# Kernel tuning notes

Hardware: AMD Instinct MI355X
Metric: run time of the kernel (lower is better)

The kernel has to match this reference:

```python
import jax, jax.numpy as jnp
import numpy as np

N_NODES = 8192
N_EDGES = 65536
MUL = 16          # multiplicity of 0e and 1o irreps
NB = 16           # num_radial_basis
HID = 16          # num_radial_dimension
MAX_RADIUS = 5.0
SQRT3 = float(np.sqrt(3.0))


def soft_unit_step(x):
    # e3nn.math.soft_unit_step: exp(-1/x) for x>0 else 0 (grad-safe where)
    safe = jnp.where(x > 0, x, 1.0)
    return jnp.where(x > 0, jnp.exp(-1.0 / safe), 0.0)


def setup_inputs() -> dict:
    key = jax.random.key(0)
    ks = jax.random.split(key, 12)
    f_in = jax.random.normal(ks[0], (N_NODES, 4 * MUL), jnp.float32)
    edge_vec = jax.random.normal(ks[1], (N_EDGES, 3), jnp.float32) * 1.5
    edge_src = jax.random.randint(ks[2], (N_EDGES,), 0, N_NODES)
    edge_dst = jax.random.randint(ks[3], (N_EDGES,), 0, N_NODES)
    Wq0 = jax.random.normal(ks[4], (MUL, MUL), jnp.float32)
    Wq1 = jax.random.normal(ks[5], (MUL, MUL), jnp.float32)
    Wk1 = jax.random.normal(ks[6], (NB, HID), jnp.float32)
    Wk2 = jax.random.normal(ks[7], (HID, 4 * MUL * MUL), jnp.float32)
    Wv1 = jax.random.normal(ks[8], (NB, HID), jnp.float32)
    Wv2 = jax.random.normal(ks[9], (HID, 4 * MUL * MUL), jnp.float32)
    Wd0 = jax.random.normal(ks[10], (MUL, MUL), jnp.float32)
    Wd1 = jax.random.normal(ks[11], (MUL, MUL), jnp.float32)
    return dict(f_in=f_in, edge_vec=edge_vec, edge_src=edge_src, edge_dst=edge_dst,
                Wq0=Wq0, Wq1=Wq1, Wk1=Wk1, Wk2=Wk2, Wv1=Wv1, Wv2=Wv2, Wd0=Wd0, Wd1=Wd1)


def _forward(f_in, edge_vec, edge_src, edge_dst,
             Wq0, Wq1, Wk1, Wk2, Wv1, Wv2, Wd0, Wd1):
    f0 = f_in[:, :MUL]                         # [N, MUL]    0e scalars
    f1 = f_in[:, MUL:].reshape(-1, MUL, 3)     # [N, MUL, 3] 1o vectors

    r = jnp.linalg.norm(edge_vec, axis=1)      # [E]
    u = edge_vec / r[:, None]
    sh1 = SQRT3 * u                            # Y_1, component norm (|Y1|^2 = 3); Y_0 = 1

    # soft_one_hot_linspace, basis='smooth_finite', cutoff=True, * sqrt(NB)
    values = jnp.linspace(0.0, MAX_RADIUS, NB + 2)
    step = values[1] - values[0]
    diff = (r[:, None] - values[1:-1]) / step
    C = 1.14136 * float(np.exp(2.0))
    rb = (C * soft_unit_step(diff + 1.0) * soft_unit_step(1.0 - diff)) * np.sqrt(NB)

    edge_cut = soft_unit_step(10.0 * (1.0 - r / MAX_RADIUS))  # [E]

    def mlp(x, W1, W2):  # e3nn FullyConnectedNet with fan-in normalization
        h = jax.nn.silu(x @ (W1 / np.sqrt(NB)))
        return h @ (W2 / np.sqrt(HID))

    wk = mlp(rb, Wk1, Wk2).reshape(-1, 4, MUL, MUL)  # per-edge TP weights
    wv = mlp(rb, Wv1, Wv2).reshape(-1, 4, MUL, MUL)

    # h_q: per-irrep linear
    q0 = f0 @ Wq0 / np.sqrt(MUL)
    q1 = jnp.einsum('nic,io->noc', f1, Wq1) / np.sqrt(MUL)

    x0 = f0[edge_src]   # [E, MUL]
    x1 = f1[edge_src]   # [E, MUL, 3]

    def fctp(w):
        # FullyConnectedTensorProduct (16x0e+16x1o) x (0e+1o) -> (16x0e+16x1o)
        # 4 paths: 0x0->0, 1x1->0 (dot/sqrt3), 0x1->1, 1x0->1
        a = 1.0 / np.sqrt(2 * MUL)
        o0 = jnp.einsum('eij,ei->ej', w[:, 0], x0) \
           + jnp.einsum('eij,eic,ec->ej', w[:, 1], x1, sh1) / SQRT3
        o1 = jnp.einsum('eij,ei,ec->ejc', w[:, 2], x0, sh1) \
           + jnp.einsum('eij,eic->ejc', w[:, 3], x1)
        return o0 * a, o1 * a

    k0, k1 = fctp(wk)
    v0, v1 = fctp(wv)

    # dot_product: FCTP(query, key) -> 0e
    ad = 1.0 / np.sqrt(2.0 * MUL * MUL)
    dot = ad * (jnp.einsum('ij,ei,ej->e', Wd0, q0[edge_dst], k0)
                + jnp.einsum('ij,eic,ejc->e', Wd1, q1[edge_dst], k1) / SQRT3)

    exp = edge_cut * jnp.exp(dot)                                   # [E]
    z = jax.ops.segment_sum(exp, edge_dst, num_segments=N_NODES)    # [N]
    z = jnp.where(z == 0.0, 1.0, z)
    alpha = exp / z[edge_dst]
    # alpha.relu().sqrt() with grad-safe sqrt at 0
    s = jnp.where(alpha > 0, jnp.sqrt(jnp.where(alpha > 0, alpha, 1.0)), 0.0)

    f_out0 = jax.ops.segment_sum(s[:, None] * v0, edge_dst, num_segments=N_NODES)
    f_out1 = jax.ops.segment_sum(s[:, None, None] * v1, edge_dst, num_segments=N_NODES)
    return jnp.concatenate([f_out0, f_out1.reshape(-1, MUL * 3)], axis=-1)  # [N, 64]


def reference(f_in, edge_vec, edge_src, edge_dst,
              Wq0, Wq1, Wk1, Wk2, Wv1, Wv2, Wd0, Wd1):
    return _forward(f_in, edge_vec, edge_src, edge_dst,
                    Wq0, Wq1, Wk1, Wk2, Wv1, Wv2, Wd0, Wd1)
```

## Files before the change

### kernel.cpp

```cpp
#include <hip/hip_runtime.h>
#include <hip/hip_bf16.h>

#define N_NODES 8192
#define N_EDGES 65536
#define BUCKET  48

#define CNT_OFF  0
#define WF_OFF   8192
#define QDI_OFF  24576
#define EXP_OFF  548864
#define VH_OFF   942080

typedef _Float16 half8 __attribute__((ext_vector_type(8)));
typedef float f32x4 __attribute__((ext_vector_type(4)));

__device__ __forceinline__ float sus_f(float x) { return x > 0.f ? __expf(-1.f / x) : 0.f; }
__device__ __forceinline__ float silu_f(float x) { return x / (1.f + __expf(-x)); }

__device__ __forceinline__ half8 vmul(half8 v, _Float16 s) {
    half8 r;
#pragma unroll
    for (int d = 0; d < 8; ++d) r[d] = v[d] * s;
    return r;
}

__global__ __launch_bounds__(256) void k_prep(
    const float* __restrict__ f_in,
    const float* __restrict__ Wq0, const float* __restrict__ Wq1,
    const float* __restrict__ Wd0, const float* __restrict__ Wd1,
    const float* __restrict__ Wk2, const float* __restrict__ Wv2,
    half8* __restrict__ wfrag, float* __restrict__ qdi, int* __restrict__ cnt) {
    __shared__ float f0s[16][16];
    __shared__ float f1s[16][48];
    __shared__ float t0s[16][16];
    __shared__ float t1s[16][48];
    const int blk = blockIdx.x;
    const int tid = threadIdx.x;

    if (blk < 16) {
        int g = blk * 256 + tid;
        int lane = g & 63, t = (g >> 6) & 7, b = (g >> 9) & 3, kv = g >> 11;
        const float* src = kv ? Wv2 : Wk2;
        int n = lane & 15, quad = lane >> 4;
        const float SC = 0.044194173824159216f;
        half8 out;
#pragma unroll
        for (int d = 0; d < 8; ++d) {
            int k = t * 32 + quad * 8 + d;
            int i = k & 15, h = k >> 4;
            out[d] = (_Float16)(src[h * 1024 + b * 256 + i * 16 + n] * SC);
        }
        wfrag[g] = out;
        return;
    }
    if (blk == 16) {
        int4 z = {0, 0, 0, 0};
#pragma unroll
        for (int i = 0; i < 8; ++i) ((int4*)cnt)[tid * 8 + i] = z;
    }
    const int j = tid & 15, ln = tid >> 4;
    const int n = (blk - 16) * 16 + ln;
    f0s[ln][j]         = f_in[n * 64 + j];
    f1s[ln][j * 3 + 0] = f_in[n * 64 + 16 + j * 3 + 0];
    f1s[ln][j * 3 + 1] = f_in[n * 64 + 16 + j * 3 + 1];
    f1s[ln][j * 3 + 2] = f_in[n * 64 + 16 + j * 3 + 2];
    __syncthreads();
    float t0 = 0.f, ta = 0.f, tb = 0.f, tc = 0.f;
#pragma unroll
    for (int p = 0; p < 16; ++p) {
        float wq0 = Wq0[p * 16 + j];
        float wq1 = Wq1[p * 16 + j];
        t0 += f0s[ln][p] * wq0;
        ta += f1s[ln][p * 3 + 0] * wq1;
        tb += f1s[ln][p * 3 + 1] * wq1;
        tc += f1s[ln][p * 3 + 2] * wq1;
    }
    t0s[ln][j] = t0;
    t1s[ln][j * 3 + 0] = ta; t1s[ln][j * 3 + 1] = tb; t1s[ln][j * 3 + 2] = tc;
    __syncthreads();
    float q0a = 0.f, qa = 0.f, qb = 0.f, qc = 0.f;
#pragma unroll
    for (int i = 0; i < 16; ++i) {
        float wd0 = Wd0[i * 16 + j];
        float wd1 = Wd1[i * 16 + j];
        q0a += t0s[ln][i] * wd0;
        qa  += t1s[ln][i * 3 + 0] * wd1;
        qb  += t1s[ln][i * 3 + 1] * wd1;
        qc  += t1s[ln][i * 3 + 2] * wd1;
    }
    const float S0 = 0.011048543456f;
    const float S1 = 0.0063788674817f;
    float4 q = {q0a * S0, qa * S1, qb * S1, qc * S1};
    ((float4*)qdi)[n * 16 + j] = q;
}

__global__ __launch_bounds__(256) void k_edge(
    const float* __restrict__ f_in, const float* __restrict__ evec,
    const int* __restrict__ esrc, const int* __restrict__ edst,
    const float* __restrict__ Wk1, const float* __restrict__ Wv1,
    const half8* __restrict__ wfrag,
    const float* __restrict__ qdi,
    int* __restrict__ cursor, float* __restrict__ expbuf, _Float16* __restrict__ vh) {
    __shared__ __align__(16) char s_arena[16384];
    _Float16 (*s_x0h)[24] = (_Float16(*)[24])(s_arena);
    _Float16 (*s_x1h0)[24] = (_Float16(*)[24])(s_arena + 3072);
    _Float16 (*s_x1h1)[24] = (_Float16(*)[24])(s_arena + 6144);
    _Float16 (*s_x1h2)[24] = (_Float16(*)[24])(s_arena + 9216);
    _Float16 (*s_hkh)[16] = (_Float16(*)[16])(s_arena + 12288);
    _Float16 (*s_hvh)[16] = (_Float16(*)[16])(s_arena + 14336);
    _Float16 (*s_vt)[72]  = (_Float16(*)[72])(s_arena);
    __shared__ float s_rb[64][16];
    __shared__ float s_sh[64][4];
    __shared__ int   s_slot[64];

    const int tid = threadIdx.x;
    const int e0 = blockIdx.x * 64;

    {
        const int el = tid >> 2, q = tid & 3;
        const int e = e0 + el;
        float v0 = evec[e * 3 + 0];
        float v1 = evec[e * 3 + 1];
        float v2 = evec[e * 3 + 2];
        float r = sqrtf(v0 * v0 + v1 * v1 + v2 * v2);
        float rs = r * 3.4f;
#pragma unroll
        for (int bb = 0; bb < 4; ++bb) {
            int b = q * 4 + bb;
            s_rb[el][b] = 33.734292f * sus_f(rs - (float)b) * sus_f((float)(b + 2) - rs);
        }
        if (q == 0) {
            float inv = r > 0.f ? 1.f / r : 0.f;
            const float SQ3 = 1.7320508075688772f;
            s_sh[el][0] = SQ3 * v0 * inv;
            s_sh[el][1] = SQ3 * v1 * inv;
            s_sh[el][2] = SQ3 * v2 * inv;
            s_sh[el][3] = sus_f(10.f - 2.f * r);
        }
    }
    __syncthreads();

    {
        const int j = tid & 15, slot = tid >> 4;
        _Float16* xp = (_Float16*)(s_arena + 3072);
#pragma unroll
        for (int s = 0; s < 4; ++s) {
            const int el = slot * 4 + s;
            const int e = e0 + el;
            float aK = 0.f, aV = 0.f;
#pragma unroll
            for (int b = 0; b < 16; ++b) {
                float rbv = s_rb[el][b];
                aK += rbv * Wk1[b * 16 + j];
                aV += rbv * Wv1[b * 16 + j];
            }
            s_hkh[el][(j & 1) * 8 + (j >> 1)] = (_Float16)silu_f(aK * 0.25f);
            s_hvh[el][(j & 1) * 8 + (j >> 1)] = (_Float16)silu_f(aV * 0.25f);
            const int src = esrc[e];
            float4 v4 = ((const float4*)f_in)[src * 16 + j];
            if (j < 4) {
#pragma unroll
                for (int d = 0; d < 4; ++d)
                    s_x0h[el][j * 4 + d] = (_Float16)((&v4.x)[d]);
            } else {
                const int cc = j * 4 - 16;
#pragma unroll
                for (int d = 0; d < 4; ++d) {
                    int c = cc + d;
                    int i = c / 3, comp = c - 3 * i;
                    xp[comp * 1536 + el * 24 + i] = (_Float16)((&v4.x)[d]);
                }
            }
        }
    }
    __syncthreads();

    const int lane = tid & 63;
    const int wv = tid >> 6;
    const int m = lane & 15, quad = lane >> 4;
    const int eb = wv * 16;
    const int eloc = eb + m;
    const int ihalf = quad >> 1;
    const int hh = (quad & 1) * 8;

    half8 X0 = *(const half8*)&s_x0h[eloc][hh];
    half8 Xa = *(const half8*)&s_x1h0[eloc][hh];
    half8 Xb = *(const half8*)&s_x1h1[eloc][hh];
    half8 Xc = *(const half8*)&s_x1h2[eloc][hh];
    half8 HK = *(const half8*)&s_hkh[eloc][ihalf * 8];
    half8 HV = *(const half8*)&s_hvh[eloc][ihalf * 8];
    half8 XS;
    {
        _Float16 u0 = (_Float16)(s_sh[eloc][0] * 0.57735026919f);
        _Float16 u1 = (_Float16)(s_sh[eloc][1] * 0.57735026919f);
        _Float16 u2 = (_Float16)(s_sh[eloc][2] * 0.57735026919f);
#pragma unroll
        for (int d = 0; d < 8; ++d) XS[d] = Xa[d] * u0 + Xb[d] * u1 + Xc[d] * u2;
    }
    __syncthreads();

    {
        int dsts[4];
        float4 qv[4];
#pragma unroll
        for (int r = 0; r < 4; ++r) {
            const int e = e0 + eb + quad * 4 + r;
            dsts[r] = edst[e];
            qv[r] = ((const float4*)qdi)[dsts[r] * 16 + m];
        }
        f32x4 o0 = {0.f, 0.f, 0.f, 0.f}, a1 = o0, ax = o0, ay = o0, az = o0;
#pragma unroll
        for (int t = 0; t < 8; ++t) {
            _Float16 hs = HK[t];
            half8 B0 = wfrag[(0 * 8 + t) * 64 + lane];
            half8 B1 = wfrag[(1 * 8 + t) * 64 + lane];
            half8 B2 = wfrag[(2 * 8 + t) * 64 + lane];
            half8 B3 = wfrag[(3 * 8 + t) * 64 + lane];
            half8 A0 = vmul(X0, hs);
            half8 As = vmul(XS, hs);
            half8 Aa = vmul(Xa, hs);
            half8 Ab = vmul(Xb, hs);
            half8 Ac = vmul(Xc, hs);
            o0 = __builtin_amdgcn_mfma_f32_16x16x32_f16(A0, B0, o0, 0, 0, 0);
            o0 = __builtin_amdgcn_mfma_f32_16x16x32_f16(As, B1, o0, 0, 0, 0);
            a1 = __builtin_amdgcn_mfma_f32_16x16x32_f16(A0, B2, a1, 0, 0, 0);
            ax = __builtin_amdgcn_mfma_f32_16x16x32_f16(Aa, B3, ax, 0, 0, 0);
            ay = __builtin_amdgcn_mfma_f32_16x16x32_f16(Ab, B3, ay, 0, 0, 0);
            az = __builtin_amdgcn_mfma_f32_16x16x32_f16(Ac, B3, az, 0, 0, 0);
        }
        const int j = m;
#pragma unroll
        for (int r = 0; r < 4; ++r) {
            const int el = eb + quad * 4 + r;
            float sh0 = s_sh[el][0], sh1 = s_sh[el][1], sh2 = s_sh[el][2];
            float k1x = a1[r] * sh0 + ax[r];
            float k1y = a1[r] * sh1 + ay[r];
            float k1z = a1[r] * sh2 + az[r];
            float4 q = qv[r];
            float dp = q.x * o0[r] + q.y * k1x + q.z * k1y + q.w * k1z;
            dp += __shfl_xor(dp, 1);
            dp += __shfl_xor(dp, 2);
            dp += __shfl_xor(dp, 4);
            dp += __shfl_xor(dp, 8);
            if (j == 0) {
                float ev = s_sh[el][3] * __expf(dp);
                int local = atomicAdd(cursor + dsts[r], 1);
                int slot = dsts[r] * BUCKET + local;
                s_slot[el] = slot;
                expbuf[slot] = ev;
            }
        }
    }

    {
        f32x4 o0 = {0.f, 0.f, 0.f, 0.f}, a1 = o0, ax = o0, ay = o0, az = o0;
        const half8* wfv = wfrag + 32 * 64;
#pragma unroll
        for (int t = 0; t < 8; ++t) {
            _Float16 hs = HV[t];
            half8 B0 = wfv[(0 * 8 + t) * 64 + lane];
            half8 B1 = wfv[(1 * 8 + t) * 64 + lane];
            half8 B2 = wfv[(2 * 8 + t) * 64 + lane];
            half8 B3 = wfv[(3 * 8 + t) * 64 + lane];
            half8 A0 = vmul(X0, hs);
            half8 As = vmul(XS, hs);
            half8 Aa = vmul(Xa, hs);
            half8 Ab = vmul(Xb, hs);
            half8 Ac = vmul(Xc, hs);
            o0 = __builtin_amdgcn_mfma_f32_16x16x32_f16(A0, B0, o0, 0, 0, 0);
            o0 = __builtin_amdgcn_mfma_f32_16x16x32_f16(As, B1, o0, 0, 0, 0);
            a1 = __builtin_amdgcn_mfma_f32_16x16x32_f16(A0, B2, a1, 0, 0, 0);
            ax = __builtin_amdgcn_mfma_f32_16x16x32_f16(Aa, B3, ax, 0, 0, 0);
            ay = __builtin_amdgcn_mfma_f32_16x16x32_f16(Ab, B3, ay, 0, 0, 0);
            az = __builtin_amdgcn_mfma_f32_16x16x32_f16(Ac, B3, az, 0, 0, 0);
        }
        const int j = m;
#pragma unroll
        for (int r = 0; r < 4; ++r) {
            const int el = eb + quad * 4 + r;
            float sh0 = s_sh[el][0], sh1 = s_sh[el][1], sh2 = s_sh[el][2];
            s_vt[el][j] = (_Float16)o0[r];
            s_vt[el][16 + j * 3 + 0] = (_Float16)(a1[r] * sh0 + ax[r]);
            s_vt[el][16 + j * 3 + 1] = (_Float16)(a1[r] * sh1 + ay[r]);
            s_vt[el][16 + j * 3 + 2] = (_Float16)(a1[r] * sh2 + az[r]);
        }
    }
    __syncthreads();

#pragma unroll
    for (int pass = 0; pass < 2; ++pass) {
        int row = pass * 32 + (tid >> 3);
        int part = tid & 7;
        half8 val = *(const half8*)&s_vt[row][part * 8];
        int slot = s_slot[row];
        *(half8*)(vh + (size_t)slot * 64 + part * 8) = val;
    }
}

__global__ __launch_bounds__(256) void k_out(
    const int* __restrict__ cnt,
    const float* __restrict__ expbuf, const _Float16* __restrict__ vh,
    float* __restrict__ fout) {
    const int col = threadIdx.x & 63;
    const int n = blockIdx.x * 4 + (threadIdx.x >> 6);
    const int deg = cnt[n];
    const int s0 = n * BUCKET;
    float zs = 0.f;
    float acc = 0.f;
    for (int i = 0; i < deg; ++i) {
        float ev = expbuf[s0 + i];
        zs += ev;
        acc += sqrtf(ev) * (float)vh[(size_t)(s0 + i) * 64 + col];
    }
    float scale = zs > 0.f ? rsqrtf(zs) : 0.f;
    fout[n * 64 + col] = acc * scale;
}

extern "C" void kernel_launch(void* const* d_in, const int* in_sizes, int n_in,
                              void* d_out, int out_size, void* d_ws, size_t ws_size,
                              hipStream_t stream) {
    const float* f_in = (const float*)d_in[0];
    const float* evec = (const float*)d_in[1];
    const int* esrc = (const int*)d_in[2];
    const int* edst = (const int*)d_in[3];
    const float* Wq0 = (const float*)d_in[4];
    const float* Wq1 = (const float*)d_in[5];
    const float* Wk1 = (const float*)d_in[6];
    const float* Wk2 = (const float*)d_in[7];
    const float* Wv1 = (const float*)d_in[8];
    const float* Wv2 = (const float*)d_in[9];
    const float* Wd0 = (const float*)d_in[10];
    const float* Wd1 = (const float*)d_in[11];

    float* ws     = (float*)d_ws;
    int*   cnt    = (int*)(ws + CNT_OFF);
    half8* wfrag  = (half8*)(ws + WF_OFF);
    float* qdi    = ws + QDI_OFF;
    float* expb   = ws + EXP_OFF;
    _Float16* vh  = (_Float16*)(ws + VH_OFF);
    float* fout   = (float*)d_out;

    k_prep<<<528, 256, 0, stream>>>(f_in, Wq0, Wq1, Wd0, Wd1, Wk2, Wv2, wfrag, qdi, cnt);
    k_edge<<<N_EDGES / 64, 256, 0, stream>>>(f_in, evec, esrc, edst, Wk1, Wv1,
                                             wfrag, qdi, cnt, expb, vh);
    k_out<<<N_NODES / 4, 256, 0, stream>>>(cnt, expb, vh, fout);
}
```

Baseline: 110.2 us.

## Fuse output aggregation into edge kernel via per-node completion counters

Degrees are now precomputed in the prep kernel, and the separate output kernel is removed. The edge kernel publishes its exp values and value rows with agent-scope atomic stores, then bumps a per-destination done counter. The block that completes a node's last edge does that node's normalised aggregation. This saves a kernel launch and the global barrier between edge and output phases. In exchange it adds a memset, more atomics, a thread fence, and uneven per-block tail work. Correctness relies on memory ordering that the relaxed stores plus the fence are meant to provide.

```diff
diff --git a/kernel.cpp b/kernel.cpp
--- a/kernel.cpp
+++ b/kernel.cpp
@@ -6,10 +6,12 @@
 #define BUCKET  48
 
 #define CNT_OFF  0
-#define WF_OFF   8192
-#define QDI_OFF  24576
-#define EXP_OFF  548864
-#define VH_OFF   942080
+#define DEG_OFF  8192
+#define DONE_OFF 16384
+#define WF_OFF   24576
+#define QDI_OFF  40960
+#define EXP_OFF  565248
+#define VH_OFF   1089536
 
 typedef _Float16 half8 __attribute__((ext_vector_type(8)));
 typedef float f32x4 __attribute__((ext_vector_type(4)));
@@ -29,7 +31,9 @@
     const float* __restrict__ Wq0, const float* __restrict__ Wq1,
     const float* __restrict__ Wd0, const float* __restrict__ Wd1,
     const float* __restrict__ Wk2, const float* __restrict__ Wv2,
-    half8* __restrict__ wfrag, float* __restrict__ qdi, int* __restrict__ cnt) {
+    const int* __restrict__ edst,
+    half8* __restrict__ wfrag, float* __restrict__ qdi,
+    int* __restrict__ deg, float* __restrict__ fout) {
     __shared__ float f0s[16][16];
     __shared__ float f1s[16][48];
     __shared__ float t0s[16][16];
@@ -53,13 +57,17 @@
         wfrag[g] = out;
         return;
     }
-    if (blk == 16) {
-        int4 z = {0, 0, 0, 0};
-#pragma unroll
-        for (int i = 0; i < 8; ++i) ((int4*)cnt)[tid * 8 + i] = z;
+    if (blk >= 528) {
+        int base = (blk - 528) * 256 + tid;
+#pragma unroll
+        for (int k = 0; k < 4; ++k) atomicAdd(deg + edst[base + k * 16384], 1);
+        return;
     }
     const int j = tid & 15, ln = tid >> 4;
-    const int n = (blk - 16) * 16 + ln;
+    const int nb = (blk - 16) * 16;
+    const int n = nb + ln;
+    float4 z4 = {0.f, 0.f, 0.f, 0.f};
+    ((float4*)fout)[nb * 16 + tid] = z4;
     f0s[ln][j]         = f_in[n * 64 + j];
     f1s[ln][j * 3 + 0] = f_in[n * 64 + 16 + j * 3 + 0];
     f1s[ln][j * 3 + 1] = f_in[n * 64 + 16 + j * 3 + 1];
@@ -100,7 +108,9 @@
     const float* __restrict__ Wk1, const float* __restrict__ Wv1,
     const half8* __restrict__ wfrag,
     const float* __restrict__ qdi,
-    int* __restrict__ cursor, float* __restrict__ expbuf, _Float16* __restrict__ vh) {
+    int* __restrict__ cursor, int* __restrict__ deg, int* __restrict__ done,
+    float* __restrict__ expbuf, _Float16* __restrict__ vh,
+    float* __restrict__ fout) {
     __shared__ __align__(16) char s_arena[16384];
     _Float16 (*s_x0h)[24] = (_Float16(*)[24])(s_arena);
     _Float16 (*s_x1h0)[24] = (_Float16(*)[24])(s_arena + 3072);
@@ -112,9 +122,12 @@
     __shared__ float s_rb[64][16];
     __shared__ float s_sh[64][4];
     __shared__ int   s_slot[64];
+    __shared__ int   s_ready[64];
+    __shared__ int   s_nready;
 
     const int tid = threadIdx.x;
     const int e0 = blockIdx.x * 64;
+    if (tid == 0) s_nready = 0;
 
     {
         const int el = tid >> 2, q = tid & 3;
@@ -245,9 +258,9 @@
             if (j == 0) {
                 float ev = s_sh[el][3] * __expf(dp);
                 int local = atomicAdd(cursor + dsts[r], 1);
-                int slot = dsts[r] * BUCKET + local;
-                s_slot[el] = slot;
-                expbuf[slot] = ev;
+                s_slot[el] = dsts[r] * BUCKET + local;
+                __hip_atomic_store(expbuf + dsts[r] * 64 + local, ev,
+                                   __ATOMIC_RELAXED, __HIP_MEMORY_SCOPE_AGENT);
             }
         }
     }
@@ -291,29 +304,40 @@
     for (int pass = 0; pass < 2; ++pass) {
         int row = pass * 32 + (tid >> 3);
         int part = tid & 7;
-        half8 val = *(const half8*)&s_vt[row][part * 8];
-        int slot = s_slot[row];
-        *(half8*)(vh + (size_t)slot * 64 + part * 8) = val;
-    }
-}
-
-__global__ __launch_bounds__(256) void k_out(
-    const int* __restrict__ cnt,
-    const float* __restrict__ expbuf, const _Float16* __restrict__ vh,
-    float* __restrict__ fout) {
-    const int col = threadIdx.x & 63;
-    const int n = blockIdx.x * 4 + (threadIdx.x >> 6);
-    const int deg = cnt[n];
-    const int s0 = n * BUCKET;
-    float zs = 0.f;
-    float acc = 0.f;
-    for (int i = 0; i < deg; ++i) {
-        float ev = expbuf[s0 + i];
-        zs += ev;
-        acc += sqrtf(ev) * (float)vh[(size_t)(s0 + i) * 64 + col];
-    }
-    float scale = zs > 0.f ? rsqrtf(zs) : 0.f;
-    fout[n * 64 + col] = acc * scale;
+        union { half8 h; unsigned long long u[2]; } cvt;
+        cvt.h = *(const half8*)&s_vt[row][part * 8];
+        unsigned long long* dst8 =
+            (unsigned long long*)(vh + (size_t)s_slot[row] * 64 + part * 8);
+        __hip_atomic_store(dst8 + 0, cvt.u[0], __ATOMIC_RELAXED, __HIP_MEMORY_SCOPE_AGENT);
+        __hip_atomic_store(dst8 + 1, cvt.u[1], __ATOMIC_RELAXED, __HIP_MEMORY_SCOPE_AGENT);
+    }
+    __syncthreads();
+
+    if (wv == 0) {
+        __threadfence();
+        const int dst = edst[e0 + lane];
+        int old = atomicAdd(done + dst, 1);
+        if (old + 1 == deg[dst]) {
+            int idx = atomicAdd(&s_nready, 1);
+            s_ready[idx] = dst;
+        }
+    }
+    __syncthreads();
+
+    const int nr = s_nready;
+    for (int i = wv; i < nr; i += 4) {
+        const int n = s_ready[i];
+        const int dn = deg[n];
+        float zs = 0.f, acc = 0.f;
+        for (int p = 0; p < dn; ++p) {
+            float ev = __hip_atomic_load(expbuf + n * 64 + p,
+                                         __ATOMIC_RELAXED, __HIP_MEMORY_SCOPE_AGENT);
+            zs += ev;
+            acc += sqrtf(ev) * (float)vh[(size_t)(n * BUCKET + p) * 64 + lane];
+        }
+        float scale = zs > 0.f ? rsqrtf(zs) : 0.f;
+        fout[n * 64 + lane] = acc * scale;
+    }
 }
 
 extern "C" void kernel_launch(void* const* d_in, const int* in_sizes, int n_in,
@@ -334,14 +358,18 @@
 
     float* ws     = (float*)d_ws;
     int*   cnt    = (int*)(ws + CNT_OFF);
+    int*   deg    = (int*)(ws + DEG_OFF);
+    int*   done   = (int*)(ws + DONE_OFF);
     half8* wfrag  = (half8*)(ws + WF_OFF);
     float* qdi    = ws + QDI_OFF;
     float* expb   = ws + EXP_OFF;
     _Float16* vh  = (_Float16*)(ws + VH_OFF);
     float* fout   = (float*)d_out;
 
-    k_prep<<<528, 256, 0, stream>>>(f_in, Wq0, Wq1, Wd0, Wd1, Wk2, Wv2, wfrag, qdi, cnt);
+    hipMemsetAsync(ws, 0, (size_t)3 * 8192 * sizeof(int), stream);
+
+    k_prep<<<592, 256, 0, stream>>>(f_in, Wq0, Wq1, Wd0, Wd1, Wk2, Wv2, edst,
+                                    wfrag, qdi, deg, fout);
     k_edge<<<N_EDGES / 64, 256, 0, stream>>>(f_in, evec, esrc, edst, Wk1, Wv1,
-                                             wfrag, qdi, cnt, expb, vh);
-    k_out<<<N_NODES / 4, 256, 0, stream>>>(cnt, expb, vh, fout);
+                                             wfrag, qdi, cnt, deg, done, expb, vh, fout);
 }
```

After: 187.3 us. +69.9%, slower.
